# Performance work log

Hardware: AMD Instinct MI355X
Metric: run time of the kernel (lower is better)

## Reference

```python
import jax, jax.numpy as jnp
import numpy as np

B, C, H, W = 16, 256, 128, 128
INTER = C // 2  # NLBlockND default inter_channels = in_channels // 2
BN_EPS = 1e-5


def setup_inputs() -> dict:
    key = jax.random.key(0)
    ks = jax.random.split(key, 14)
    s = lambda n: 1.0 / np.sqrt(n)
    inp = {
        'x':  jax.random.normal(ks[0], (B, C, H, W), jnp.float32),
        # NLBlockND 1x1 convs (spatial input is 1x1 after avg-pool -> matmuls)
        'Wg': jax.random.normal(ks[1], (INTER, C), jnp.float32) * s(C),
        'bg': jax.random.normal(ks[2], (INTER,), jnp.float32) * s(C),
        'Wt': jax.random.normal(ks[3], (INTER, C), jnp.float32) * s(C),
        'bt': jax.random.normal(ks[4], (INTER,), jnp.float32) * s(C),
        'Wp': jax.random.normal(ks[5], (INTER, C), jnp.float32) * s(C),
        'bp': jax.random.normal(ks[6], (INTER,), jnp.float32) * s(C),
        'Wf': jax.random.normal(ks[7], (1, 2 * INTER), jnp.float32) * s(2 * INTER),
        'bf': jax.random.normal(ks[8], (1,), jnp.float32) * s(2 * INTER),
        'Wz': jax.random.normal(ks[9], (C, INTER), jnp.float32) * s(INTER),
        'bz': jax.random.normal(ks[10], (C,), jnp.float32) * s(INTER),
        'gamma': jax.random.normal(ks[11], (C,), jnp.float32),
        'beta':  jax.random.normal(ks[12], (C,), jnp.float32),
        # eca_layer_two: Conv2d(C, 1, kernel_size=1, bias=False)
        'W3': jax.random.normal(ks[13], (1, C), jnp.float32) * s(C),
    }
    return inp


def reference(x, Wg, bg, Wt, bt, Wp, bp, Wf, bf, Wz, bz, gamma, beta, W3):
    b = x.shape[0]
    # ---- nonlocal_layer: avg-pool -> NLBlockND('concatenate') on 1x1 map ----
    p = jnp.mean(x, axis=(2, 3))                      # [b, C] pooled vector
    g_x = p @ Wg.T + bg                               # [b, INTER]
    th  = p @ Wt.T + bt                               # theta  [b, INTER]
    ph  = p @ Wp.T + bp                               # phi    [b, INTER]
    cat = jnp.concatenate([th, ph], axis=1)           # [b, 2*INTER]
    f = jax.nn.relu(cat @ Wf.T + bf)                  # [b, 1]; N=1 so f_div_C = f
    y = f * g_x                                       # [b, INTER]
    wy = y @ Wz.T + bz                                # [b, C]
    # BatchNorm2d (training mode, spatial=1x1): stats over batch per channel
    mu = jnp.mean(wy, axis=0)
    var = jnp.var(wy, axis=0)
    bn = gamma * (wy - mu) * jax.lax.rsqrt(var + BN_EPS) + beta
    z = bn + p                                        # residual
    scores = jax.nn.sigmoid(z)                        # [b, C]
    # top-3 channel selection, then per-sample gather of channels from x
    _, idx = jax.lax.top_k(scores, 3)                 # [b, 3]
    x1 = jnp.take_along_axis(x, idx[:, :, None, None], axis=1)  # [b, 3, H, W]
    # ---- eca_layer_two: 1x1 conv C->1 (no bias) + exact GELU ----
    x3 = jax.nn.gelu(jnp.einsum('bchw,oc->bohw', x, W3), approximate=False)  # [b,1,H,W]
    # conv2 (eca_layer_one) output is discarded (x2 = zeros_like, unused)
    return jnp.concatenate([x3, x1], axis=1)          # [b, 4, H, W]
```

## Files before the change

kernel.cpp:

```cpp
#include <hip/hip_runtime.h>

#define HW    16384
#define NCH   256
#define NB    16
#define INTER 128
#define HW4   4096


__global__ __launch_bounds__(256) void k_pool_x3(
    const float* __restrict__ x, const float* __restrict__ W3, float* out)
{
    const int tile = blockIdx.x;
    const int b    = blockIdx.y;
    const int tid  = threadIdx.x;
    const int wave = tid >> 6, lane = tid & 63;

    __shared__ float w3f[NCH];
    __shared__ float wsum[4][NCH];
    w3f[tid] = W3[tid];
    __syncthreads();

    const int p4 = tile * 256 + tid;
    const float4* xb = (const float4*)x + (size_t)b * NCH * HW4 + p4;

    float4 bufA[8], bufB[8];
    float a0 = 0.f, a1 = 0.f, a2 = 0.f, a3 = 0.f;

    #pragma unroll
    for (int j = 0; j < 8; ++j) bufA[j] = xb[(size_t)j * HW4];

    #define PROCESS(BUF, CBASE)                                             \
        _Pragma("unroll")                                                   \
        for (int j = 0; j < 8; ++j) {                                       \
            const int c = (CBASE) + j;                                      \
            float4 v = BUF[j];                                              \
            float w = w3f[c];                                               \
            a0 = fmaf(v.x, w, a0); a1 = fmaf(v.y, w, a1);                   \
            a2 = fmaf(v.z, w, a2); a3 = fmaf(v.w, w, a3);                   \
            float cs = (v.x + v.y) + (v.z + v.w);                           \
            cs += __shfl_xor(cs, 1);                                        \
            cs += __shfl_xor(cs, 2);                                        \
            cs += __shfl_xor(cs, 4);                                        \
            cs += __shfl_xor(cs, 8);                                        \
            cs += __shfl_xor(cs, 16);                                       \
            cs += __shfl_xor(cs, 32);                                       \
            if (lane == 0) wsum[wave][c] = cs;                              \
        }

    for (int cb = 0; cb < 32; cb += 2) {
        #pragma unroll
        for (int j = 0; j < 8; ++j) bufB[j] = xb[(size_t)((cb + 1) * 8 + j) * HW4];
        PROCESS(bufA, cb * 8)
        if (cb + 2 < 32) {
            #pragma unroll
            for (int j = 0; j < 8; ++j) bufA[j] = xb[(size_t)((cb + 2) * 8 + j) * HW4];
        }
        PROCESS(bufB, (cb + 1) * 8)
    }
    #undef PROCESS

    __syncthreads();
    float s = wsum[0][tid] + wsum[1][tid] + wsum[2][tid] + wsum[3][tid];
    out[(size_t)(b * 4 + 1) * HW + tile * NCH + tid] = s;

    const float is2 = 0.70710678118654752440f;
    float4 g;
    g.x = 0.5f * a0 * (1.f + erff(a0 * is2));
    g.y = 0.5f * a1 * (1.f + erff(a1 * is2));
    g.z = 0.5f * a2 * (1.f + erff(a2 * is2));
    g.w = 0.5f * a3 * (1.f + erff(a3 * is2));
    ((float4*)out)[(size_t)b * 4 * HW4 + p4] = g;
}

__global__ __launch_bounds__(256) void k_mlp(
    const float* outbuf,
    const float* __restrict__ Wg, const float* __restrict__ bg,
    const float* __restrict__ Wt, const float* __restrict__ bt,
    const float* __restrict__ Wp, const float* __restrict__ bp,
    const float* __restrict__ Wf, const float* __restrict__ bfv,
    const float* __restrict__ Wz, const float* __restrict__ bz,
    float* __restrict__ p_out, float* __restrict__ wy_out)
{
    const int b = blockIdx.x, tid = threadIdx.x;
    __shared__ float sp[NCH];
    __shared__ float sg[INTER], sth[INTER], sph[INTER];
    __shared__ float red[NCH];
    __shared__ float sy[INTER];
    __shared__ float sf;

    const float* psum = outbuf + (size_t)(b * 4 + 1) * HW;
    float s = 0.f;
    #pragma unroll
    for (int t = 0; t < 16; ++t) s += psum[t * NCH + tid];
    float pv = s * (1.0f / 16384.0f);
    sp[tid] = pv;
    p_out[b * NCH + tid] = pv;
    __syncthreads();

    for (int j = tid; j < 3 * INTER; j += 256) {
        const float* Wrow; float bias; int i, which;
        if (j < INTER)        { i = j;           Wrow = Wg + i * NCH; bias = bg[i]; which = 0; }
        else if (j < 2*INTER) { i = j - INTER;   Wrow = Wt + i * NCH; bias = bt[i]; which = 1; }
        else                  { i = j - 2*INTER; Wrow = Wp + i * NCH; bias = bp[i]; which = 2; }
        float acc = bias;
        for (int k = 0; k < NCH; k += 4) {
            float4 q = *(const float4*)(Wrow + k);
            acc = fmaf(q.x, sp[k+0], acc);
            acc = fmaf(q.y, sp[k+1], acc);
            acc = fmaf(q.z, sp[k+2], acc);
            acc = fmaf(q.w, sp[k+3], acc);
        }
        if (which == 0) sg[i] = acc;
        else if (which == 1) sth[i] = acc;
        else sph[i] = acc;
    }
    __syncthreads();

    float cat = (tid < INTER) ? sth[tid] : sph[tid - INTER];
    red[tid] = cat * Wf[tid];
    __syncthreads();
    if (tid == 0) {
        float acc = bfv[0];
        for (int k = 0; k < NCH; ++k) acc += red[k];
        sf = fmaxf(acc, 0.f);
    }
    __syncthreads();
    if (tid < INTER) sy[tid] = sf * sg[tid];
    __syncthreads();

    {
        const float* Wrow = Wz + tid * INTER;
        float acc = bz[tid];
        for (int k = 0; k < INTER; k += 4) {
            float4 q = *(const float4*)(Wrow + k);
            acc = fmaf(q.x, sy[k+0], acc);
            acc = fmaf(q.y, sy[k+1], acc);
            acc = fmaf(q.z, sy[k+2], acc);
            acc = fmaf(q.w, sy[k+3], acc);
        }
        wy_out[b * NCH + tid] = acc;
    }
}

__global__ __launch_bounds__(256) void k_bn_topk(
    const float* __restrict__ wy, const float* __restrict__ p,
    const float* __restrict__ gamma, const float* __restrict__ beta,
    int* __restrict__ sel_out)
{
    const int b = blockIdx.x, tid = threadIdx.x;
    const int wave = tid >> 6, lane = tid & 63;
    __shared__ float wsc[4];
    __shared__ int   wid[4];
    __shared__ int   sel[3];

    float vv[16];
    float mu = 0.f;
    #pragma unroll
    for (int bb = 0; bb < 16; ++bb) { vv[bb] = wy[bb * NCH + tid]; mu += vv[bb]; }
    mu *= (1.f / 16.f);
    float var = 0.f;
    #pragma unroll
    for (int bb = 0; bb < 16; ++bb) { float d = vv[bb] - mu; var = fmaf(d, d, var); }
    var *= (1.f / 16.f);

    float bn = gamma[tid] * (vv[b] - mu) * rsqrtf(var + 1e-5f) + beta[tid];
    float z  = bn + p[b * NCH + tid];
    float sc = 1.f / (1.f + expf(-z));

    for (int r = 0; r < 3; ++r) {
        float s = sc; int id = tid;
        #pragma unroll
        for (int m = 1; m <= 32; m <<= 1) {
            float so = __shfl_xor(s, m);
            int   io = __shfl_xor(id, m);
            if (so > s || (so == s && io < id)) { s = so; id = io; }
        }
        if (lane == 0) { wsc[wave] = s; wid[wave] = id; }
        __syncthreads();
        if (tid == 0) {
            float bs = wsc[0]; int bi = wid[0];
            for (int w = 1; w < 4; ++w)
                if (wsc[w] > bs || (wsc[w] == bs && wid[w] < bi)) { bs = wsc[w]; bi = wid[w]; }
            sel[r] = bi;
        }
        __syncthreads();
        if (tid == sel[r]) sc = -1e30f;
        __syncthreads();
    }
    if (tid < 3) sel_out[b * 3 + tid] = sel[tid];
}

__global__ __launch_bounds__(256) void k_gather(
    const float* __restrict__ x, const int* __restrict__ sel,
    float* __restrict__ out)
{
    const int seg = blockIdx.x;
    const int r   = blockIdx.y;
    const int b   = blockIdx.z;
    const int ch  = sel[b * 3 + r];
    const float4* src = (const float4*)x + (size_t)(b * NCH + ch) * HW4 + seg * 1024;
    float4*       dst = (float4*)out + (size_t)(b * 4 + 1 + r) * HW4 + seg * 1024;
    #pragma unroll
    for (int i = 0; i < 4; ++i)
        dst[i * 256 + threadIdx.x] = src[i * 256 + threadIdx.x];
}

extern "C" void kernel_launch(void* const* d_in, const int* in_sizes, int n_in,
                              void* d_out, int out_size, void* d_ws, size_t ws_size,
                              hipStream_t stream)
{
    const float* x     = (const float*)d_in[0];
    const float* Wg    = (const float*)d_in[1];
    const float* bg    = (const float*)d_in[2];
    const float* Wt    = (const float*)d_in[3];
    const float* bt    = (const float*)d_in[4];
    const float* Wp    = (const float*)d_in[5];
    const float* bp    = (const float*)d_in[6];
    const float* Wf    = (const float*)d_in[7];
    const float* bfv   = (const float*)d_in[8];
    const float* Wz    = (const float*)d_in[9];
    const float* bz    = (const float*)d_in[10];
    const float* gamma = (const float*)d_in[11];
    const float* beta  = (const float*)d_in[12];
    const float* W3    = (const float*)d_in[13];
    float* out = (float*)d_out;

    float* wy  = (float*)d_ws;
    float* p   = wy + NB * NCH;
    int*   sel = (int*)(p + NB * NCH);

    k_pool_x3<<<dim3(16, 16), 256, 0, stream>>>(x, W3, out);
    k_mlp<<<NB, 256, 0, stream>>>(out, Wg, bg, Wt, bt, Wp, bp, Wf, bfv, Wz, bz, p, wy);
    k_bn_topk<<<NB, 256, 0, stream>>>(wy, p, gamma, beta, sel);
    k_gather<<<dim3(4, 3, NB), 256, 0, stream>>>(x, sel, out);
}
```

Measured before the change: 419.9 us.

## Split channels across eight waves in pool/conv kernel with LDS cross-wave reduction

The fused pool+1x1-conv kernel now uses 512 threads, and each wave owns a 32-channel slice instead of every wave walking all 256 channels. Each lane handles four float4 pixel groups, so the per-channel spatial sum needs only one shuffle plus a strided LDS table instead of a six-step shuffle tree per channel. Partial conv accumulators from the eight waves are combined through shared memory by wave 0, which then applies GELU. This cuts shuffle work and raises parallelism per block, at the cost of much larger LDS use (about 64KB) and an extra reduction phase serialized on one wave.

After: 396.1 us. 5.7% less time.

```diff
diff --git a/kernel.cpp b/kernel.cpp
--- a/kernel.cpp
+++ b/kernel.cpp
@@ -5,71 +5,111 @@
 #define NB    16
 #define INTER 128
 #define HW4   4096
-
-
-__global__ __launch_bounds__(256) void k_pool_x3(
+#define WSTR  34
+
+
+__global__ __launch_bounds__(512, 2) void k_pool_x3(
     const float* __restrict__ x, const float* __restrict__ W3, float* out)
 {
     const int tile = blockIdx.x;
     const int b    = blockIdx.y;
     const int tid  = threadIdx.x;
     const int wave = tid >> 6, lane = tid & 63;
-
-    __shared__ float w3f[NCH];
-    __shared__ float wsum[4][NCH];
-    w3f[tid] = W3[tid];
-    __syncthreads();
-
-    const int p4 = tile * 256 + tid;
-    const float4* xb = (const float4*)x + (size_t)b * NCH * HW4 + p4;
+    const int c0   = wave << 5;
+
+    __shared__ float  w3f[NCH];
+    __shared__ float  wsum[NCH * WSTR];
+    __shared__ float4 comb[7][256];
+
+    if (tid < NCH) w3f[tid] = W3[tid];
+    __syncthreads();
+
+    const float4* xb = (const float4*)x + (size_t)b * NCH * HW4
+                     + (size_t)c0 * HW4 + tile * 256 + lane;
+
+    float4 a[4];
+    #pragma unroll
+    for (int q = 0; q < 4; ++q) a[q] = make_float4(0.f, 0.f, 0.f, 0.f);
 
     float4 bufA[8], bufB[8];
-    float a0 = 0.f, a1 = 0.f, a2 = 0.f, a3 = 0.f;
-
-    #pragma unroll
-    for (int j = 0; j < 8; ++j) bufA[j] = xb[(size_t)j * HW4];
+    #pragma unroll
+    for (int j = 0; j < 8; ++j)
+        bufA[j] = xb[(size_t)(j >> 2) * HW4 + (j & 3) * 64];
 
     #define PROCESS(BUF, CBASE)                                             \
         _Pragma("unroll")                                                   \
-        for (int j = 0; j < 8; ++j) {                                       \
-            const int c = (CBASE) + j;                                      \
-            float4 v = BUF[j];                                              \
-            float w = w3f[c];                                               \
-            a0 = fmaf(v.x, w, a0); a1 = fmaf(v.y, w, a1);                   \
-            a2 = fmaf(v.z, w, a2); a3 = fmaf(v.w, w, a3);                   \
-            float cs = (v.x + v.y) + (v.z + v.w);                           \
-            cs += __shfl_xor(cs, 1);                                        \
-            cs += __shfl_xor(cs, 2);                                        \
-            cs += __shfl_xor(cs, 4);                                        \
-            cs += __shfl_xor(cs, 8);                                        \
-            cs += __shfl_xor(cs, 16);                                       \
+        for (int h = 0; h < 2; ++h) {                                       \
+            const int c = (CBASE) + h;                                      \
+            const float w = w3f[c0 + c];                                    \
+            float cs = 0.f;                                                 \
+            _Pragma("unroll")                                               \
+            for (int q = 0; q < 4; ++q) {                                   \
+                float4 v = BUF[h * 4 + q];                                  \
+                a[q].x = fmaf(v.x, w, a[q].x);                              \
+                a[q].y = fmaf(v.y, w, a[q].y);                              \
+                a[q].z = fmaf(v.z, w, a[q].z);                              \
+                a[q].w = fmaf(v.w, w, a[q].w);                              \
+                cs += (v.x + v.y) + (v.z + v.w);                            \
+            }                                                               \
             cs += __shfl_xor(cs, 32);                                       \
-            if (lane == 0) wsum[wave][c] = cs;                              \
-        }
-
-    for (int cb = 0; cb < 32; cb += 2) {
-        #pragma unroll
-        for (int j = 0; j < 8; ++j) bufB[j] = xb[(size_t)((cb + 1) * 8 + j) * HW4];
-        PROCESS(bufA, cb * 8)
-        if (cb + 2 < 32) {
+            if (lane < 32) wsum[(c0 + c) * WSTR + lane] = cs;               \
+        }
+
+    for (int cc = 0; cc < 32; cc += 4) {
+        #pragma unroll
+        for (int j = 0; j < 8; ++j)
+            bufB[j] = xb[(size_t)(cc + 2 + (j >> 2)) * HW4 + (j & 3) * 64];
+        PROCESS(bufA, cc)
+        if (cc + 4 < 32) {
             #pragma unroll
-            for (int j = 0; j < 8; ++j) bufA[j] = xb[(size_t)((cb + 2) * 8 + j) * HW4];
-        }
-        PROCESS(bufB, (cb + 1) * 8)
+            for (int j = 0; j < 8; ++j)
+                bufA[j] = xb[(size_t)(cc + 4 + (j >> 2)) * HW4 + (j & 3) * 64];
+        }
+        PROCESS(bufB, cc + 2)
     }
     #undef PROCESS
 
     __syncthreads();
-    float s = wsum[0][tid] + wsum[1][tid] + wsum[2][tid] + wsum[3][tid];
-    out[(size_t)(b * 4 + 1) * HW + tile * NCH + tid] = s;
-
-    const float is2 = 0.70710678118654752440f;
-    float4 g;
-    g.x = 0.5f * a0 * (1.f + erff(a0 * is2));
-    g.y = 0.5f * a1 * (1.f + erff(a1 * is2));
-    g.z = 0.5f * a2 * (1.f + erff(a2 * is2));
-    g.w = 0.5f * a3 * (1.f + erff(a3 * is2));
-    ((float4*)out)[(size_t)b * 4 * HW4 + p4] = g;
+
+    {
+        const int ch = tid >> 1, half = tid & 1;
+        const float* rowp = &wsum[ch * WSTR + half * 16];
+        float s = 0.f;
+        #pragma unroll
+        for (int k = 0; k < 8; ++k) {
+            float2 v2 = *(const float2*)(rowp + k * 2);
+            s += v2.x + v2.y;
+        }
+        s += __shfl_xor(s, 1);
+        if (half == 0)
+            out[(size_t)(b * 4 + 1) * HW + tile * NCH + ch] = s;
+    }
+
+    if (wave > 0) {
+        #pragma unroll
+        for (int q = 0; q < 4; ++q) comb[wave - 1][q * 64 + lane] = a[q];
+    }
+    __syncthreads();
+    if (wave == 0) {
+        #pragma unroll
+        for (int j = 0; j < 7; ++j) {
+            #pragma unroll
+            for (int q = 0; q < 4; ++q) {
+                float4 v = comb[j][q * 64 + lane];
+                a[q].x += v.x; a[q].y += v.y; a[q].z += v.z; a[q].w += v.w;
+            }
+        }
+        const float is2 = 0.70710678118654752440f;
+        #pragma unroll
+        for (int q = 0; q < 4; ++q) {
+            float4 r;
+            r.x = 0.5f * a[q].x * (1.f + erff(a[q].x * is2));
+            r.y = 0.5f * a[q].y * (1.f + erff(a[q].y * is2));
+            r.z = 0.5f * a[q].z * (1.f + erff(a[q].z * is2));
+            r.w = 0.5f * a[q].w * (1.f + erff(a[q].w * is2));
+            ((float4*)out)[(size_t)b * 4 * HW4 + tile * 256 + q * 64 + lane] = r;
+        }
+    }
 }
 
 __global__ __launch_bounds__(256) void k_mlp(
@@ -229,7 +269,7 @@
     float* p   = wy + NB * NCH;
     int*   sel = (int*)(p + NB * NCH);
 
-    k_pool_x3<<<dim3(16, 16), 256, 0, stream>>>(x, W3, out);
+    k_pool_x3<<<dim3(16, 16), 512, 0, stream>>>(x, W3, out);
     k_mlp<<<NB, 256, 0, stream>>>(out, Wg, bg, Wt, bt, Wp, bp, Wf, bfv, Wz, bz, p, wy);
     k_bn_topk<<<NB, 256, 0, stream>>>(wy, p, gamma, beta, sel);
     k_gather<<<dim3(4, 3, NB), 256, 0, stream>>>(x, sel, out);
```
